# Kernel optimization log

Hardware: AMD Instinct MI355X
Metric: run time of the kernel (lower is better)

The kernel has to match this reference:

```python
import jax, jax.numpy as jnp
import numpy as np

V, D, H, B, T = 50000, 256, 512, 64, 512
FORGET_BIAS = 1.0  # TF LSTMCell default

def setup_inputs() -> dict:
    key = jax.random.key(0)
    k1, k2, k3, k4 = jax.random.split(key, 4)
    word_indices = jax.random.randint(k1, (B, T), 0, V, dtype=jnp.int32)
    num_words = jax.random.randint(k2, (B,), 1, T + 1, dtype=jnp.int32)
    # Embedding: uniform(-1, 1) per original
    W_emb = jax.random.uniform(k3, (V, D), minval=-1.0, maxval=1.0, dtype=jnp.float32)
    # TF LSTMCell: single kernel [(D+H), 4H] with gate order i, j, f, o; zero bias
    kernel = jax.random.normal(k4, (D + H, 4 * H), dtype=jnp.float32) * 0.02
    bias = jnp.zeros((4 * H,), dtype=jnp.float32)
    return {"word_indices": word_indices, "num_words": num_words,
            "W_emb": W_emb, "kernel": kernel, "bias": bias}

def reference(word_indices, num_words, W_emb, kernel, bias):
    # embedding lookup: [B, T, D]
    x = W_emb[word_indices]
    xs = jnp.swapaxes(x, 0, 1)  # [T, B, D] time-major
    ts = jnp.arange(xs.shape[0])
    c0 = jnp.zeros((word_indices.shape[0], H), dtype=x.dtype)
    h0 = jnp.zeros_like(c0)

    def step(carry, inp):
        c, h = carry
        x_t, t = inp
        gates = jnp.concatenate([x_t, h], axis=-1) @ kernel + bias  # [B, 4H]
        i, j, f, o = jnp.split(gates, 4, axis=-1)
        c_new = jax.nn.sigmoid(f + FORGET_BIAS) * c + jax.nn.sigmoid(i) * jnp.tanh(j)
        h_new = jax.nn.sigmoid(o) * jnp.tanh(c_new)
        # static_rnn sequence_length semantics: copy state through past the end
        mask = (t < num_words)[:, None]
        c = jnp.where(mask, c_new, c)
        h = jnp.where(mask, h_new, h)
        return (c, h), None

    (c_fin, h_fin), _ = jax.lax.scan(step, (c0, h0), (xs, ts))
    # TF LSTM final_state = LSTMStateTuple(c, h); stack for a single array output
    return jnp.stack([c_fin, h_fin], axis=0)  # [2, B, H]
```

## Files before the change

kernel.cpp:

```cpp
#include <hip/hip_runtime.h>
#include <stdint.h>


#define NWG     64
#define NTHR    256
#define TSTEPS  512
#define BATCH   64
#define EDIM    256
#define HID     512
#define GCOLS   2048

typedef __attribute__((ext_vector_type(8))) short short8;
typedef __attribute__((ext_vector_type(4))) float f32x4;


__device__ __forceinline__ unsigned short f2bf(float f) {
  unsigned u = __float_as_uint(f);
  unsigned r = (u + 0x7FFFu + ((u >> 16) & 1u)) >> 16;
  return (unsigned short)r;
}
__device__ __forceinline__ float sigf(float x) {
  x = fminf(fmaxf(x, -30.0f), 30.0f);
  return 1.0f / (1.0f + __expf(-x));
}
__device__ __forceinline__ float tanh_fast(float x) {
  x = fminf(fmaxf(x, -15.0f), 15.0f);
  float e = __expf(-2.0f * x);
  return (1.0f - e) / (1.0f + e);
}
__device__ __forceinline__ void lstm_cell(float gi, float gj, float gf, float go,
                                          int t, int nw, float& c, float& h) {
  float cn = sigf(gf + 1.0f) * c + sigf(gi) * tanh_fast(gj);
  float hn = sigf(go) * tanh_fast(cn);
  if (t < nw) { c = cn; h = hn; }
}

__global__ void init_ws(unsigned* ws, int nwords) {
  int i = blockIdx.x * 256 + threadIdx.x;
  if (i < nwords) ws[i] = 0u;
}

__global__ void embed_k(const int* __restrict__ widx, const float* __restrict__ Wemb,
                        unsigned short* __restrict__ xb) {
  int tb = blockIdx.x;
  int t = tb >> 6, b = tb & 63;
  int wi = widx[b * TSTEPS + t];
  const float* src = Wemb + (size_t)wi * EDIM + threadIdx.x * 4;
  float4 v = *(const float4*)src;
  ushort4 o;
  o.x = f2bf(v.x); o.y = f2bf(v.y); o.z = f2bf(v.z); o.w = f2bf(v.w);
  *(ushort4*)(xb + (size_t)tb * EDIM + threadIdx.x * 4) = o;
}

__launch_bounds__(NTHR, 1)
__global__ void lstm_persist(const int* __restrict__ num_words,
                             const int* __restrict__ widx,
                             const float* __restrict__ Wemb,
                             const float* __restrict__ Wk,
                             const float* __restrict__ bias,
                             const unsigned short* __restrict__ xb,
                             unsigned short* __restrict__ hb0,
                             unsigned short* __restrict__ hb1,
                             unsigned* flags,
                             float* __restrict__ out,
                             int has_xb)
{
  __shared__ alignas(16) short Wlds[24576];

  const int tid  = threadIdx.x;
  const int lane = tid & 63;
  const int wv   = tid >> 6;
  const int u0   = blockIdx.x * 8;

  for (int q = tid; q < 3072; q += NTHR) {
    int lq = q & 63;
    int kkn = q >> 6;
    int nt = (kkn >= 24) ? 1 : 0;
    int kk = kkn - nt * 24;
    int kbase = kk * 32 + ((lq >> 4) << 3);
    int nn = (nt << 4) + (lq & 15);
    int gcol = ((nn >> 3) << 9) + u0 + (nn & 7);
    short8 v;
#pragma unroll
    for (int j = 0; j < 8; ++j)
      v[j] = (short)f2bf(Wk[(size_t)(kbase + j) * GCOLS + gcol]);
    *(short8*)&Wlds[q * 8] = v;
  }

  const int n   = lane & 15;
  const int q4  = lane >> 4;
  const int bb  = wv * 16 + n;
  const int kq  = q4 << 3;
  const int un  = n & 7;
  const bool lo = (n < 8);

  float bias_g[4];
#pragma unroll
  for (int g = 0; g < 4; ++g) bias_g[g] = bias[g * HID + u0 + un];
  int nw_r[4];
#pragma unroll
  for (int r = 0; r < 4; ++r) nw_r[r] = num_words[wv * 16 + q4 * 4 + r];

  float c_r[4] = {0.f, 0.f, 0.f, 0.f};
  float h_r[4] = {0.f, 0.f, 0.f, 0.f};

  unsigned* myflag = flags + ((blockIdx.x << 2) + wv) * 32;
  const unsigned* fp = flags + ((lane << 2) + wv) * 32;

  unsigned short* hb[2] = {hb0, hb1};

  __syncthreads();

  for (int t = 0; t < TSTEPS; ++t) {
    f32x4 acc0 = {0.f, 0.f, 0.f, 0.f};
    f32x4 acc1 = {0.f, 0.f, 0.f, 0.f};

    if (has_xb) {
      const unsigned short* xrow = xb + ((size_t)t * BATCH + bb) * EDIM + kq;
#pragma unroll
      for (int kk = 0; kk < 8; ++kk) {
        short8 a  = __builtin_bit_cast(short8, *(const uint4*)(xrow + kk * 32));
        short8 w0 = *(const short8*)&Wlds[((kk)      * 64 + lane) * 8];
        short8 w1 = *(const short8*)&Wlds[((24 + kk) * 64 + lane) * 8];
        acc0 = __builtin_amdgcn_mfma_f32_16x16x32_bf16(a, w0, acc0, 0, 0, 0);
        acc1 = __builtin_amdgcn_mfma_f32_16x16x32_bf16(a, w1, acc1, 0, 0, 0);
      }
    } else {
      int wi = widx[bb * TSTEPS + t];
      const float* erow = Wemb + (size_t)wi * EDIM + kq;
#pragma unroll
      for (int kk = 0; kk < 8; ++kk) {
        float4 f0 = *(const float4*)(erow + kk * 32);
        float4 f1 = *(const float4*)(erow + kk * 32 + 4);
        short8 a;
        a[0] = (short)f2bf(f0.x); a[1] = (short)f2bf(f0.y);
        a[2] = (short)f2bf(f0.z); a[3] = (short)f2bf(f0.w);
        a[4] = (short)f2bf(f1.x); a[5] = (short)f2bf(f1.y);
        a[6] = (short)f2bf(f1.z); a[7] = (short)f2bf(f1.w);
        short8 w0 = *(const short8*)&Wlds[((kk)      * 64 + lane) * 8];
        short8 w1 = *(const short8*)&Wlds[((24 + kk) * 64 + lane) * 8];
        acc0 = __builtin_amdgcn_mfma_f32_16x16x32_bf16(a, w0, acc0, 0, 0, 0);
        acc1 = __builtin_amdgcn_mfma_f32_16x16x32_bf16(a, w1, acc1, 0, 0, 0);
      }
    }

    if (t > 0) {
      const unsigned tgt = (unsigned)t;
      for (;;) {
        unsigned v;
        asm volatile("global_load_dword %0, %1, off sc0 sc1\n\t"
                     "s_waitcnt vmcnt(0)" : "=v"(v) : "v"(fp));
        if (__ballot(v >= tgt) == ~0ull) break;
      }

      const unsigned short* hr = hb[t & 1] + bb * HID + kq;
      uint4 av[16];
#pragma unroll
      for (int kk = 0; kk < 16; ++kk)
        asm volatile("global_load_dwordx4 %0, %1, off sc0 sc1"
                     : "=v"(av[kk]) : "v"(hr + kk * 32));
      asm volatile("s_waitcnt vmcnt(0)" ::: "memory");
      __builtin_amdgcn_sched_barrier(0);
#pragma unroll
      for (int kk = 0; kk < 16; ++kk) {
        short8 a  = __builtin_bit_cast(short8, av[kk]);
        short8 w0 = *(const short8*)&Wlds[((8 + kk)  * 64 + lane) * 8];
        short8 w1 = *(const short8*)&Wlds[((32 + kk) * 64 + lane) * 8];
        acc0 = __builtin_amdgcn_mfma_f32_16x16x32_bf16(a, w0, acc0, 0, 0, 0);
        acc1 = __builtin_amdgcn_mfma_f32_16x16x32_bf16(a, w1, acc1, 0, 0, 0);
      }
    }

#pragma unroll
    for (int r = 0; r < 4; ++r) {
      float a0o = acc0[r], a1o = acc1[r];
      float a0x = __shfl_xor(a0o, 8);
      float a1x = __shfl_xor(a1o, 8);
      float gi = lo ? a0o : a0x;
      float gj = lo ? a0x : a0o;
      float gf = lo ? a1o : a1x;
      float go = lo ? a1x : a1o;
      lstm_cell(gi + bias_g[0], gj + bias_g[1], gf + bias_g[2], go + bias_g[3],
                t, nw_r[r], c_r[r], h_r[r]);
    }

    if (t + 1 < TSTEPS) {
      unsigned short* hw = hb[(t + 1) & 1];
      if (lo) {
#pragma unroll
        for (int r = 0; r < 4; ++r) {
          unsigned short* dst = hw + (size_t)(wv * 16 + q4 * 4 + r) * HID + u0 + un;
          unsigned hv = (unsigned)f2bf(h_r[r]);
          asm volatile("global_store_short %0, %1, off sc0 sc1"
                       :: "v"(dst), "v"(hv) : "memory");
        }
      }
      asm volatile("s_waitcnt vmcnt(0)" ::: "memory");
      if (lane == 0) {
        unsigned fv = (unsigned)(t + 1);
        asm volatile("global_store_dword %0, %1, off sc0 sc1"
                     :: "v"(myflag), "v"(fv) : "memory");
      }
    }
  }

  if (lo) {
#pragma unroll
    for (int r = 0; r < 4; ++r) {
      int b = wv * 16 + q4 * 4 + r;
      out[b * HID + u0 + un]                   = c_r[r];
      out[BATCH * HID + b * HID + u0 + un]     = h_r[r];
    }
  }
}

extern "C" void kernel_launch(void* const* d_in, const int* in_sizes, int n_in,
                              void* d_out, int out_size, void* d_ws, size_t ws_size,
                              hipStream_t stream) {
  const int*   widx = (const int*)d_in[0];
  const int*   nw   = (const int*)d_in[1];
  const float* Wemb = (const float*)d_in[2];
  const float* Wk   = (const float*)d_in[3];
  const float* bias = (const float*)d_in[4];
  float* out = (float*)d_out;
  char* ws = (char*)d_ws;

  unsigned* flags       = (unsigned*)(ws + 256);
  unsigned short* hb0   = (unsigned short*)(ws + 33280);
  unsigned short* hb1   = (unsigned short*)(ws + 98816);
  unsigned short* xb    = (unsigned short*)(ws + 164352);

  size_t need = 164352ull + (size_t)TSTEPS * BATCH * EDIM * 2;
  int has_xb = (ws_size >= need) ? 1 : 0;

  const int init_words = 164352 / 4;
  init_ws<<<(init_words + 255) / 256, 256, 0, stream>>>((unsigned*)ws, init_words);
  if (has_xb)
    embed_k<<<TSTEPS * BATCH, 64, 0, stream>>>(widx, Wemb, xb);

  void* args[] = {(void*)&nw, (void*)&widx, (void*)&Wemb, (void*)&Wk, (void*)&bias,
                  (void*)&xb, (void*)&hb0, (void*)&hb1, (void*)&flags,
                  (void*)&out, (void*)&has_xb};
  hipLaunchCooperativeKernel((void*)lstm_persist, dim3(NWG), dim3(NTHR), args, 0, stream);
}
```

Before: 2.558 ms.

## Prefetch next-step embeddings, overlap x-GEMM with h loads, coalesce h stores via LDS

```diff
diff --git a/kernel.cpp b/kernel.cpp
--- a/kernel.cpp
+++ b/kernel.cpp
@@ -66,6 +66,7 @@
                              int has_xb)
 {
   __shared__ alignas(16) short Wlds[24576];
+  __shared__ alignas(16) unsigned short hstg[1024];
 
   const int tid  = threadIdx.x;
   const int lane = tid & 63;
@@ -109,40 +110,32 @@
 
   unsigned short* hb[2] = {hb0, hb1};
 
+  float4 pfw[16];
+  uint4  pfx[8];
+  auto PREFETCH = [&](int tt) {
+    if (has_xb) {
+      const unsigned short* xrow = xb + ((size_t)tt * BATCH + bb) * EDIM + kq;
+#pragma unroll
+      for (int kk = 0; kk < 8; ++kk)
+        pfx[kk] = *(const uint4*)(xrow + kk * 32);
+    } else {
+      int wi = widx[bb * TSTEPS + tt];
+      const float* er = Wemb + (size_t)wi * EDIM + kq;
+#pragma unroll
+      for (int kk = 0; kk < 8; ++kk) {
+        pfw[2 * kk]     = *(const float4*)(er + kk * 32);
+        pfw[2 * kk + 1] = *(const float4*)(er + kk * 32 + 4);
+      }
+    }
+  };
+  PREFETCH(0);
+
   __syncthreads();
 
   for (int t = 0; t < TSTEPS; ++t) {
     f32x4 acc0 = {0.f, 0.f, 0.f, 0.f};
     f32x4 acc1 = {0.f, 0.f, 0.f, 0.f};
-
-    if (has_xb) {
-      const unsigned short* xrow = xb + ((size_t)t * BATCH + bb) * EDIM + kq;
-#pragma unroll
-      for (int kk = 0; kk < 8; ++kk) {
-        short8 a  = __builtin_bit_cast(short8, *(const uint4*)(xrow + kk * 32));
-        short8 w0 = *(const short8*)&Wlds[((kk)      * 64 + lane) * 8];
-        short8 w1 = *(const short8*)&Wlds[((24 + kk) * 64 + lane) * 8];
-        acc0 = __builtin_amdgcn_mfma_f32_16x16x32_bf16(a, w0, acc0, 0, 0, 0);
-        acc1 = __builtin_amdgcn_mfma_f32_16x16x32_bf16(a, w1, acc1, 0, 0, 0);
-      }
-    } else {
-      int wi = widx[bb * TSTEPS + t];
-      const float* erow = Wemb + (size_t)wi * EDIM + kq;
-#pragma unroll
-      for (int kk = 0; kk < 8; ++kk) {
-        float4 f0 = *(const float4*)(erow + kk * 32);
-        float4 f1 = *(const float4*)(erow + kk * 32 + 4);
-        short8 a;
-        a[0] = (short)f2bf(f0.x); a[1] = (short)f2bf(f0.y);
-        a[2] = (short)f2bf(f0.z); a[3] = (short)f2bf(f0.w);
-        a[4] = (short)f2bf(f1.x); a[5] = (short)f2bf(f1.y);
-        a[6] = (short)f2bf(f1.z); a[7] = (short)f2bf(f1.w);
-        short8 w0 = *(const short8*)&Wlds[((kk)      * 64 + lane) * 8];
-        short8 w1 = *(const short8*)&Wlds[((24 + kk) * 64 + lane) * 8];
-        acc0 = __builtin_amdgcn_mfma_f32_16x16x32_bf16(a, w0, acc0, 0, 0, 0);
-        acc1 = __builtin_amdgcn_mfma_f32_16x16x32_bf16(a, w1, acc1, 0, 0, 0);
-      }
-    }
+    uint4 av[16];
 
     if (t > 0) {
       const unsigned tgt = (unsigned)t;
@@ -152,13 +145,32 @@
                      "s_waitcnt vmcnt(0)" : "=v"(v) : "v"(fp));
         if (__ballot(v >= tgt) == ~0ull) break;
       }
-
       const unsigned short* hr = hb[t & 1] + bb * HID + kq;
-      uint4 av[16];
 #pragma unroll
       for (int kk = 0; kk < 16; ++kk)
         asm volatile("global_load_dwordx4 %0, %1, off sc0 sc1"
                      : "=v"(av[kk]) : "v"(hr + kk * 32));
+    }
+
+#pragma unroll
+    for (int kk = 0; kk < 8; ++kk) {
+      short8 a;
+      if (has_xb) {
+        a = __builtin_bit_cast(short8, pfx[kk]);
+      } else {
+        float4 f0 = pfw[2 * kk], f1 = pfw[2 * kk + 1];
+        a[0] = (short)f2bf(f0.x); a[1] = (short)f2bf(f0.y);
+        a[2] = (short)f2bf(f0.z); a[3] = (short)f2bf(f0.w);
+        a[4] = (short)f2bf(f1.x); a[5] = (short)f2bf(f1.y);
+        a[6] = (short)f2bf(f1.z); a[7] = (short)f2bf(f1.w);
+      }
+      short8 w0 = *(const short8*)&Wlds[((kk)      * 64 + lane) * 8];
+      short8 w1 = *(const short8*)&Wlds[((24 + kk) * 64 + lane) * 8];
+      acc0 = __builtin_amdgcn_mfma_f32_16x16x32_bf16(a, w0, acc0, 0, 0, 0);
+      acc1 = __builtin_amdgcn_mfma_f32_16x16x32_bf16(a, w1, acc1, 0, 0, 0);
+    }
+
+    if (t > 0) {
       asm volatile("s_waitcnt vmcnt(0)" ::: "memory");
       __builtin_amdgcn_sched_barrier(0);
 #pragma unroll
@@ -188,14 +200,22 @@
       unsigned short* hw = hb[(t + 1) & 1];
       if (lo) {
 #pragma unroll
-        for (int r = 0; r < 4; ++r) {
-          unsigned short* dst = hw + (size_t)(wv * 16 + q4 * 4 + r) * HID + u0 + un;
-          unsigned hv = (unsigned)f2bf(h_r[r]);
-          asm volatile("global_store_short %0, %1, off sc0 sc1"
-                       :: "v"(dst), "v"(hv) : "memory");
-        }
-      }
-      asm volatile("s_waitcnt vmcnt(0)" ::: "memory");
+        for (int r = 0; r < 4; ++r)
+          hstg[wv * 256 + (q4 * 4 + r) * 8 + un] = f2bf(h_r[r]);
+      }
+      asm volatile("s_waitcnt lgkmcnt(0)" ::: "memory");
+      {
+        int row = lane >> 2, p = lane & 3;
+        unsigned hv = *(const unsigned*)&hstg[wv * 256 + row * 8 + p * 2];
+        unsigned* dst = (unsigned*)(hw + (size_t)(wv * 16 + row) * HID + u0) + p;
+        asm volatile("global_store_dword %0, %1, off sc0 sc1"
+                     :: "v"(dst), "v"(hv) : "memory");
+      }
+      PREFETCH(t + 1);
+      if (has_xb)
+        asm volatile("s_waitcnt vmcnt(8)" ::: "memory");
+      else
+        asm volatile("s_waitcnt vmcnt(16)" ::: "memory");
       if (lane == 0) {
         unsigned fv = (unsigned)(t + 1);
         asm volatile("global_store_dword %0, %1, off sc0 sc1"
@@ -241,5 +261,5 @@
   void* args[] = {(void*)&nw, (void*)&widx, (void*)&Wemb, (void*)&Wk, (void*)&bias,
                   (void*)&xb, (void*)&hb0, (void*)&hb1, (void*)&flags,
                   (void*)&out, (void*)&has_xb};
-  hipLaunchCooperativeKernel((void*)lstm_persist, dim3(NWG), dim3(NTHR), args, 0, stream);
-}
+  (void)hipLaunchCooperativeKernel((void*)lstm_persist, dim3(NWG), dim3(NTHR), args, 0, stream);
+}
```

After: 2.405 ms. -6.0%, faster.
